# Kernel optimization log

Measured on AMD Instinct MI355X. Metric: run time of the kernel, lower is better.

The kernel has to match this reference:

```python
import jax, jax.numpy as jnp
import numpy as np

NUM_CAPS = 16   # O
CAPS_DIM = 16   # D
ROUTINGS = 3


def setup_inputs() -> dict:
    key = jax.random.key(0)
    k1, k2 = jax.random.split(key)
    x = jax.random.normal(k1, (16, 32, 32, 8, 16), dtype=jnp.float32)   # [B,H,W,I,Din]
    # he_normal-ish scale for 5x5x16 fan-in
    W = jax.random.normal(k2, (5, 5, 16, NUM_CAPS * CAPS_DIM), dtype=jnp.float32) * jnp.sqrt(2.0 / (5 * 5 * 16))
    b = 0.1 * jnp.ones((1, 1, NUM_CAPS, CAPS_DIM), dtype=jnp.float32)  # constant(0.1) init
    return {"x": x, "W": W, "b": b}


def _squash(s):
    # original: (s/||s||) * (||s||^2 / (1+||s||^2))  ==  s*||s|| / (1+||s||^2)
    n2 = jnp.sum(s * s, axis=-1, keepdims=True)
    return s * jnp.sqrt(n2) / (1.0 + n2)


def reference(x, W, b):
    B, H, Wd, I, Din = x.shape
    O, D = NUM_CAPS, CAPS_DIM
    # transpose [3,0,1,2,4] -> [I,B,H,W,Din], merge caps into batch for shared conv
    xt = jnp.transpose(x, (3, 0, 1, 2, 4)).reshape(I * B, H, Wd, Din)
    conv = jax.lax.conv_general_dilated(
        xt, W, window_strides=(1, 1), padding="SAME",
        dimension_numbers=("NHWC", "HWIO", "NHWC"))
    Hc, Wc = conv.shape[1], conv.shape[2]
    # Faithful to original: flattened I-major batch reshaped as [B, I, ...]
    votes = conv.reshape(B, I, Hc, Wc, O, D)
    biases = jnp.broadcast_to(b, (Hc, Wc, O, D))  # tile b over spatial grid

    logits = jnp.zeros((B, I, Hc, Wc, O), dtype=votes.dtype)
    activation = jnp.zeros((B, Hc, Wc, O, D), dtype=votes.dtype)
    for it in range(ROUTINGS):
        route = jax.nn.softmax(logits, axis=-1)            # over output caps O
        preact = jnp.einsum('bihwo,bihwod->bhwod', route, votes) + biases
        activation = _squash(preact)                       # [B,Hc,Wc,O,D]
        if it < ROUTINGS - 1:
            # agreement: <vote, activation> summed over D
            logits = logits + jnp.einsum('bihwod,bhwod->bihwo', votes, activation)
    return activation
```

## Files before the change

### kernel.cpp

```cpp
#include <hip/hip_runtime.h>
#include <math.h>


typedef __attribute__((ext_vector_type(8))) _Float16 half8;
typedef __attribute__((ext_vector_type(4))) _Float16 half4;
typedef __attribute__((ext_vector_type(4))) float f32x4;

__global__ void prep_w(const float* __restrict__ wg, _Float16* __restrict__ bh) {
    int k = blockIdx.x;
    int n = threadIdx.x;
    float f = (k < 400) ? wg[k * 256 + n] : 0.0f;
    bh[(k >> 3) * 2048 + n * 8 + (k & 7)] = (_Float16)f;
}

template<int CTRL>
__device__ __forceinline__ float dppf(float x) {
    return __int_as_float(__builtin_amdgcn_update_dpp(
        0, __float_as_int(x), CTRL, 0xF, 0xF, true));
}
__device__ __forceinline__ float sum16(float x) {
    x += dppf<0xB1>(x);
    x += dppf<0x4E>(x);
    x += dppf<0x124>(x);
    x += dppf<0x128>(x);
    return x;
}

__global__ __launch_bounds__(256, 4) void caps_mfma_kernel(
    const float* __restrict__ xg,
    const _Float16* __restrict__ bhg,
    const float* __restrict__ bg,
    float* __restrict__ outg)
{
    __shared__ __align__(16) char buf[31232];
    __shared__ float logit_s[1024];
    __shared__ float route_s[1024];

    _Float16* xs_h = (_Float16*)buf;
    _Float16* xs_l = (_Float16*)(buf + 15616);
    float*    vt   = (float*)buf;

    const int t      = threadIdx.x;
    const int blk    = blockIdx.x;
    const int wt     = blk & 3;
    const int h0     = (blk >> 2) & 31;
    const int bp     = blk >> 7;
    const int w0base = wt << 3;
    const int i_x    = bp >> 1;
    const int bbase  = (bp & 1) << 3;

    const float bias_r = bg[t];

    const float4* x4 = (const float4*)xg;
    #pragma unroll
    for (int kk = 0; kk < 8; ++kk) {
        int idx4 = t + (kk << 8);
        if (idx4 < 1920) {
            int c2 = idx4 & 3;
            int i  = (idx4 >> 2) & 7;
            int rc = idx4 >> 5;
            int r  = rc / 12;
            int cc = rc - r * 12;
            int hh = h0 + r - 2;
            int ww = w0base + cc - 2;
            float4 f = make_float4(0.f, 0.f, 0.f, 0.f);
            if (hh >= 0 && hh < 32 && ww >= 0 && ww < 32)
                f = x4[((((bbase + i) * 32 + hh) * 32 + ww) * 8 + i_x) * 4 + c2];
            _Float16 hx = (_Float16)f.x, hy = (_Float16)f.y;
            _Float16 hz = (_Float16)f.z, hw = (_Float16)f.w;
            _Float16 lx = (_Float16)(f.x - (float)hx);
            _Float16 ly = (_Float16)(f.y - (float)hy);
            _Float16 lz = (_Float16)(f.z - (float)hz);
            _Float16 lw = (_Float16)(f.w - (float)hw);
            half4 h4, l4;
            h4.x = hx; h4.y = hy; h4.z = hz; h4.w = hw;
            l4.x = lx; l4.y = ly; l4.z = lz; l4.w = lw;
            int a = i * 976 + rc * 16 + c2 * 4;
            *(half4*)&xs_h[a] = h4;
            *(half4*)&xs_l[a] = l4;
        }
    }
    __syncthreads();

    const int wv   = t >> 6;
    const int lane = t & 63;
    const int lrow = lane & 15;
    const int h8   = lane >> 4;
    const int ia   = lrow & 7;
    const int qh   = lrow >> 3;

    f32x4 acc[4][4];
    #pragma unroll
    for (int ms = 0; ms < 4; ++ms)
        #pragma unroll
        for (int nt = 0; nt < 4; ++nt)
            acc[ms][nt] = (f32x4){0.f, 0.f, 0.f, 0.f};

    const half8* bhp = (const half8*)bhg;

#define CONV_CHUNK(CH, TAIL)                                                   \
    {                                                                          \
        int k  = (CH) * 32 + h8 * 8;                                           \
        int p  = k >> 4;                                                       \
        int kh = p / 5;                                                        \
        int kw = p - kh * 5;                                                   \
        int c0 = k & 15;                                                       \
        int abase = ia * 976 + (kh * 12 + kw + qh) * 16 + c0;                  \
        int g = (CH) * 4 + h8;                                                 \
        half8 bhv[4];                                                          \
        _Pragma("unroll")                                                      \
        for (int nt = 0; nt < 4; ++nt) {                                       \
            int n = wv * 64 + nt * 16 + lrow;                                  \
            bhv[nt] = bhp[g * 256 + n];                                        \
        }                                                                      \
        _Pragma("unroll")                                                      \
        for (int ms = 0; ms < 4; ++ms) {                                       \
            half8 ahv, alv;                                                    \
            if (!(TAIL) || h8 < 2) {                                           \
                ahv = *(const half8*)&xs_h[abase + ms * 32];                   \
                alv = *(const half8*)&xs_l[abase + ms * 32];                   \
            } else { ahv = (half8)(_Float16)0.f; alv = (half8)(_Float16)0.f; } \
            _Pragma("unroll")                                                  \
            for (int nt = 0; nt < 4; ++nt) {                                   \
                acc[ms][nt] = __builtin_amdgcn_mfma_f32_16x16x32_f16(ahv, bhv[nt], acc[ms][nt], 0, 0, 0); \
                acc[ms][nt] = __builtin_amdgcn_mfma_f32_16x16x32_f16(alv, bhv[nt], acc[ms][nt], 0, 0, 0); \
            }                                                                  \
        }                                                                      \
    }

    #pragma unroll
    for (int ch = 0; ch < 12; ++ch) CONV_CHUNK(ch, false)
    CONV_CHUNK(12, true)
#undef CONV_CHUNK

    float v[8][8];
    #pragma unroll
    for (int ms = 0; ms < 4; ++ms) {
        __syncthreads();
        #pragma unroll
        for (int nt = 0; nt < 4; ++nt) {
            int n = wv * 64 + nt * 16 + lrow;
            *(f32x4*)&vt[n * 16 + ((h8 ^ (n & 3)) << 2)] = acc[ms][nt];
        }
        __syncthreads();
        #pragma unroll
        for (int rb = 0; rb < 4; ++rb) {
            f32x4 x = *(const f32x4*)&vt[t * 16 + ((rb ^ (t & 3)) << 2)];
            int q  = ms * 2 + (rb >> 1);
            int ib = (rb & 1) * 4;
            v[q][ib + 0] = x[0];
            v[q][ib + 1] = x[1];
            v[q][ib + 2] = x[2];
            v[q][ib + 3] = x[3];
        }
    }

    const int o = t >> 4;
    const int d = t & 15;
    const bool b8  = (d & 8) != 0;
    const bool b2v = (d & 2) != 0;
    const bool b1v = (d & 1) != 0;
    const int  im  = (b8 ? 4 : 0) + (b2v ? 2 : 0) + (b1v ? 1 : 0);
    const bool wr  = (d & 4) == 0;
    float act_r[8];

    auto agree = [&](const float* vq, float act, int q, bool first) {
        float p[8];
        #pragma unroll
        for (int i = 0; i < 8; ++i) p[i] = vq[i] * act;
        float s4[4];
        #pragma unroll
        for (int j = 0; j < 4; ++j) {
            float send = b8 ? p[j] : p[j + 4];
            float rcv  = dppf<0x128>(send);
            s4[j] = (b8 ? p[j + 4] : p[j]) + rcv;
        }
        float s2[2];
        #pragma unroll
        for (int j = 0; j < 2; ++j) {
            float send = b2v ? s4[j] : s4[j + 2];
            float rcv  = dppf<0x4E>(send);
            s2[j] = (b2v ? s4[j + 2] : s4[j]) + rcv;
        }
        float send = b1v ? s2[0] : s2[1];
        float rcv  = dppf<0xB1>(send);
        float s1 = (b1v ? s2[1] : s2[0]) + rcv;
        float L = s1 + __int_as_float(
            __builtin_amdgcn_ds_swizzle(__float_as_int(s1), 0x101F));
        if (wr) {
            float* dst = &logit_s[q * 128 + im * 16 + o];
            if (first) *dst = L; else *dst += L;
        }
    };

    #pragma unroll
    for (int q = 0; q < 8; ++q) {
        float s = 0.0f;
        #pragma unroll
        for (int i = 0; i < 8; ++i) s += v[q][i];
        float pre = bias_r + 0.0625f * s;
        float n2 = sum16(pre * pre);
        float act = pre * sqrtf(n2) * __builtin_amdgcn_rcpf(1.0f + n2);
        act_r[q] = act;
        agree(v[q], act, q, true);
    }
    __syncthreads();

    #pragma unroll
    for (int it = 1; it < 3; ++it) {
        {
            int rr = t >> 2, sq = rr >> 3, si = rr & 7, sj = t & 3;
            f32x4 lg = *(const f32x4*)&logit_s[rr * 16 + sj * 4];
            float m = fmaxf(fmaxf(lg[0], lg[1]), fmaxf(lg[2], lg[3]));
            m = fmaxf(m, dppf<0xB1>(m));
            m = fmaxf(m, dppf<0x4E>(m));
            float e0 = __expf(lg[0] - m), e1 = __expf(lg[1] - m);
            float e2 = __expf(lg[2] - m), e3 = __expf(lg[3] - m);
            float ss = e0 + e1 + e2 + e3;
            ss += dppf<0xB1>(ss);
            ss += dppf<0x4E>(ss);
            float inv = __builtin_amdgcn_rcpf(ss);
            float* rt = &route_s[sq * 128 + si];
            rt[(sj * 4 + 0) * 8] = e0 * inv;
            rt[(sj * 4 + 1) * 8] = e1 * inv;
            rt[(sj * 4 + 2) * 8] = e2 * inv;
            rt[(sj * 4 + 3) * 8] = e3 * inv;
        }
        __syncthreads();

        #pragma unroll
        for (int q = 0; q < 8; ++q) {
            const f32x4* rp = (const f32x4*)&route_s[q * 128 + o * 8];
            f32x4 ra = rp[0], rb2 = rp[1];
            float pre = bias_r
                + ra[0] * v[q][0] + ra[1] * v[q][1] + ra[2] * v[q][2] + ra[3] * v[q][3]
                + rb2[0] * v[q][4] + rb2[1] * v[q][5] + rb2[2] * v[q][6] + rb2[3] * v[q][7];
            float n2 = sum16(pre * pre);
            float act = pre * sqrtf(n2) * __builtin_amdgcn_rcpf(1.0f + n2);
            act_r[q] = act;
            if (it == 1) agree(v[q], act, q, false);
        }
        if (it == 1) __syncthreads();
    }

    #pragma unroll
    for (int q = 0; q < 8; ++q)
        outg[((bp * 32 + h0) * 32 + (w0base + q)) * 256 + t] = act_r[q];
}

extern "C" void kernel_launch(void* const* d_in, const int* in_sizes, int n_in,
                              void* d_out, int out_size, void* d_ws, size_t ws_size,
                              hipStream_t stream) {
    const float* x = (const float*)d_in[0];
    const float* w = (const float*)d_in[1];
    const float* b = (const float*)d_in[2];
    float* out = (float*)d_out;

    _Float16* bh = (_Float16*)d_ws;

    hipLaunchKernelGGL(prep_w, dim3(416), dim3(256), 0, stream, w, bh);
    hipLaunchKernelGGL(caps_mfma_kernel, dim3(2048), dim3(256), 0, stream,
                       x, bh, b, out);
}
```

Measured before the change: 122.5 us.

## Fuse weight fp16 conversion into conv kernel and pad vote transpose buffer

Drops the separate prep_w launch. The main kernel now reads the fp32 weights directly as float4 rows and packs them to fp16 with cvt_pkrtz, which permutes the output-column mapping per lane to match. The LDS transpose of conv results switches from an XOR swizzle to a stride-17 padded layout. This saves a kernel launch and the workspace round trip. In exchange every block fetches twice the weight bytes from cache, adds per-chunk conversion work, and issues 16-byte LDS accesses at addresses that are not 16-byte aligned.

After: 141.6 us. 15.6% more time.

```diff
diff --git a/kernel.cpp b/kernel.cpp
--- a/kernel.cpp
+++ b/kernel.cpp
@@ -6,12 +6,8 @@
 typedef __attribute__((ext_vector_type(4))) _Float16 half4;
 typedef __attribute__((ext_vector_type(4))) float f32x4;
 
-__global__ void prep_w(const float* __restrict__ wg, _Float16* __restrict__ bh) {
-    int k = blockIdx.x;
-    int n = threadIdx.x;
-    float f = (k < 400) ? wg[k * 256 + n] : 0.0f;
-    bh[(k >> 3) * 2048 + n * 8 + (k & 7)] = (_Float16)f;
-}
+typedef decltype(__builtin_amdgcn_cvt_pkrtz(0.f, 0.f)) pk16;
+union H8U { half8 h8; pk16 h2[4]; };
 
 template<int CTRL>
 __device__ __forceinline__ float dppf(float x) {
@@ -26,9 +22,11 @@
     return x;
 }
 
+#define VTS 17
+
 __global__ __launch_bounds__(256, 4) void caps_mfma_kernel(
     const float* __restrict__ xg,
-    const _Float16* __restrict__ bhg,
+    const float* __restrict__ wg,
     const float* __restrict__ bg,
     float* __restrict__ outg)
 {
@@ -96,27 +94,36 @@
         for (int nt = 0; nt < 4; ++nt)
             acc[ms][nt] = (f32x4){0.f, 0.f, 0.f, 0.f};
 
-    const half8* bhp = (const half8*)bhg;
+    const f32x4* w4 = (const f32x4*)wg;
 
 #define CONV_CHUNK(CH, TAIL)                                                   \
     {                                                                          \
-        int k  = (CH) * 32 + h8 * 8;                                           \
-        int p  = k >> 4;                                                       \
+        int k0 = (CH) * 32 + h8 * 8;                                           \
+        int p  = k0 >> 4;                                                      \
         int kh = p / 5;                                                        \
         int kw = p - kh * 5;                                                   \
-        int c0 = k & 15;                                                       \
+        int c0 = k0 & 15;                                                      \
         int abase = ia * 976 + (kh * 12 + kw + qh) * 16 + c0;                  \
-        int g = (CH) * 4 + h8;                                                 \
+        bool bvalid = !(TAIL) || h8 < 2;                                       \
+        f32x4 wj[8];                                                           \
+        _Pragma("unroll")                                                      \
+        for (int j = 0; j < 8; ++j)                                            \
+            wj[j] = bvalid ? w4[(k0 + j) * 64 + wv * 16 + lrow]                \
+                           : (f32x4){0.f, 0.f, 0.f, 0.f};                      \
         half8 bhv[4];                                                          \
         _Pragma("unroll")                                                      \
         for (int nt = 0; nt < 4; ++nt) {                                       \
-            int n = wv * 64 + nt * 16 + lrow;                                  \
-            bhv[nt] = bhp[g * 256 + n];                                        \
+            H8U u;                                                             \
+            u.h2[0] = __builtin_amdgcn_cvt_pkrtz(wj[0][nt], wj[1][nt]);        \
+            u.h2[1] = __builtin_amdgcn_cvt_pkrtz(wj[2][nt], wj[3][nt]);        \
+            u.h2[2] = __builtin_amdgcn_cvt_pkrtz(wj[4][nt], wj[5][nt]);        \
+            u.h2[3] = __builtin_amdgcn_cvt_pkrtz(wj[6][nt], wj[7][nt]);        \
+            bhv[nt] = u.h8;                                                    \
         }                                                                      \
         _Pragma("unroll")                                                      \
         for (int ms = 0; ms < 4; ++ms) {                                       \
             half8 ahv, alv;                                                    \
-            if (!(TAIL) || h8 < 2) {                                           \
+            if (bvalid) {                                                      \
                 ahv = *(const half8*)&xs_h[abase + ms * 32];                   \
                 alv = *(const half8*)&xs_l[abase + ms * 32];                   \
             } else { ahv = (half8)(_Float16)0.f; alv = (half8)(_Float16)0.f; } \
@@ -139,13 +146,13 @@
         __syncthreads();
         #pragma unroll
         for (int nt = 0; nt < 4; ++nt) {
-            int n = wv * 64 + nt * 16 + lrow;
-            *(f32x4*)&vt[n * 16 + ((h8 ^ (n & 3)) << 2)] = acc[ms][nt];
+            int n = wv * 64 + lrow * 4 + nt;
+            *(f32x4*)&vt[n * VTS + h8 * 4] = acc[ms][nt];
         }
         __syncthreads();
         #pragma unroll
         for (int rb = 0; rb < 4; ++rb) {
-            f32x4 x = *(const f32x4*)&vt[t * 16 + ((rb ^ (t & 3)) << 2)];
+            f32x4 x = *(const f32x4*)&vt[t * VTS + rb * 4];
             int q  = ms * 2 + (rb >> 1);
             int ib = (rb & 1) * 4;
             v[q][ib + 0] = x[0];
@@ -256,9 +263,6 @@
     const float* b = (const float*)d_in[2];
     float* out = (float*)d_out;
 
-    _Float16* bh = (_Float16*)d_ws;
-
-    hipLaunchKernelGGL(prep_w, dim3(416), dim3(256), 0, stream, w, bh);
     hipLaunchKernelGGL(caps_mfma_kernel, dim3(2048), dim3(256), 0, stream,
-                       x, bh, b, out);
-}
+                       x, w, b, out);
+}
```
